# Performance work log

Measured on AMD Instinct MI355X. Metric: run time of the kernel, lower is better.

The kernel has to match this reference:

```python
import jax, jax.numpy as jnp
import numpy as np

BN_EPS = 1e-5


def segment_mean(data, ids, num_segments):
    s = jax.ops.segment_sum(data, ids, num_segments=num_segments)
    cnt = jax.ops.segment_sum(jnp.ones((data.shape[0], 1), data.dtype), ids,
                              num_segments=num_segments)
    return s / jnp.maximum(cnt, 1.0)


def sage_conv(x_src, x_dst, src, dst, Wl, Wr, b):
    # PyG SAGEConv (aggr='mean', root_weight=True):
    # out = lin_l(mean_j x_src[j]) + lin_r(x_dst)
    agg = segment_mean(x_src[src], dst, x_dst.shape[0])
    return agg @ Wl + b + x_dst @ Wr


def simple_conv(x, src, dst, W1, b1, W2, b2):
    # message = MLP(concat[x_j, x_i - x_j]); mean aggregation at target i
    x_j = x[src]
    x_i = x[dst]
    tmp = jnp.concatenate([x_j, x_i - x_j], axis=1)          # [E, 2d]
    msg = jax.nn.elu(tmp @ W1 + b1) @ W2 + b2                 # [E, d_out]
    return segment_mean(msg, dst, x.shape[0])


def batch_norm(x, gamma, beta):
    # training-mode BatchNorm1d: biased batch stats
    mu = jnp.mean(x, axis=0)
    var = jnp.mean(jnp.square(x - mu), axis=0)
    return gamma * (x - mu) * jax.lax.rsqrt(var + BN_EPS) + beta


def setup_inputs() -> dict:
    key = jax.random.key(0)
    ks = jax.random.split(key, 12)
    n_stu, n_item, d = 100000, 20000, 128
    e_r, e_p = 500000, 300000
    s = 1.0 / np.sqrt(d)
    s2 = 1.0 / np.sqrt(2 * d)
    return {
        "x_student": jax.random.normal(ks[0], (n_stu, d), jnp.float32),
        "x_item": jax.random.normal(ks[1], (n_item, d), jnp.float32),
        "responds_src": jax.random.randint(ks[2], (e_r,), 0, n_stu),
        "responds_dst": jax.random.randint(ks[3], (e_r,), 0, n_item),
        "preceeds_src": jax.random.randint(ks[4], (e_p,), 0, n_stu),
        "preceeds_dst": jax.random.randint(ks[5], (e_p,), 0, n_stu),
        "sage_it_Wl": jax.random.normal(ks[6], (d, d), jnp.float32) * s,
        "sage_it_Wr": jax.random.normal(ks[7], (d, d), jnp.float32) * s,
        "sage_it_b": jnp.zeros((d,), jnp.float32),
        "sage_st_Wl": jax.random.normal(ks[8], (d, d), jnp.float32) * s,
        "sage_st_Wr": jax.random.normal(ks[9], (d, d), jnp.float32) * s,
        "sage_st_b": jnp.zeros((d,), jnp.float32),
        "sc_W1": jax.random.normal(ks[10], (2 * d, d), jnp.float32) * s2,
        "sc_b1": jnp.zeros((d,), jnp.float32),
        "sc_W2": jax.random.normal(ks[11], (d, d), jnp.float32) * s,
        "sc_b2": jnp.zeros((d,), jnp.float32),
        "bn_item_g": jnp.ones((d,), jnp.float32),
        "bn_item_b": jnp.zeros((d,), jnp.float32),
        "bn_stu_g": jnp.ones((d,), jnp.float32),
        "bn_stu_b": jnp.zeros((d,), jnp.float32),
    }


def reference(x_student, x_item, responds_src, responds_dst, preceeds_src,
              preceeds_dst, sage_it_Wl, sage_it_Wr, sage_it_b, sage_st_Wl,
              sage_st_Wr, sage_st_b, sc_W1, sc_b1, sc_W2, sc_b2, bn_item_g,
              bn_item_b, bn_stu_g, bn_stu_b):
    # ('student','responds','item'): SAGEConv -> item
    item_out = sage_conv(x_student, x_item, responds_src, responds_dst,
                         sage_it_Wl, sage_it_Wr, sage_it_b)
    # ('item','rev_responds','student'): SAGEConv on reversed edges -> student
    stu_sage = sage_conv(x_item, x_student, responds_dst, responds_src,
                         sage_st_Wl, sage_st_Wr, sage_st_b)
    # ('student','preceeds','student'): SimpleConv -> student
    stu_simple = simple_conv(x_student, preceeds_src, preceeds_dst,
                             sc_W1, sc_b1, sc_W2, sc_b2)
    # HeteroConv aggr='mean' over the two student contributions
    stu_out = (stu_sage + stu_simple) * 0.5

    item_out = batch_norm(jax.nn.elu(item_out), bn_item_g, bn_item_b)
    stu_out = batch_norm(jax.nn.elu(stu_out), bn_stu_g, bn_stu_b)
    return item_out, stu_out
```

## Files before the change

### kernel.cpp

```cpp
#include <hip/hip_runtime.h>
#include <hip/hip_bf16.h>
#include <math.h>

#define D 128

typedef unsigned short ushort_t;
typedef __attribute__((ext_vector_type(8))) short bf16x8;
typedef __attribute__((ext_vector_type(4))) float f32x4;

__device__ __forceinline__ float bf2f(unsigned short u) {
    union { unsigned int i; float f; } c; c.i = ((unsigned int)u) << 16; return c.f;
}
__device__ __forceinline__ unsigned short f2bf(float f) {
    union { float f; unsigned int i; } c; c.f = f;
    unsigned int x = c.i + 0x7fffu + ((c.i >> 16) & 1u);
    return (unsigned short)(x >> 16);
}
__device__ __forceinline__ float eluf(float x) { return x > 0.f ? x : (expf(x) - 1.f); }

__device__ __forceinline__ void gload_lds16(const void* g, void* l) {
    __builtin_amdgcn_global_load_lds(
        (const __attribute__((address_space(1))) unsigned int*)g,
        (__attribute__((address_space(3))) unsigned int*)l, 16, 0, 0);
}

__global__ __launch_bounds__(256) void k_setup(
    const float* __restrict__ sc_W1, const float* __restrict__ it_Wl,
    const float* __restrict__ it_Wr, const float* __restrict__ st_Wl,
    const float* __restrict__ st_Wr, const float* __restrict__ sc_W2,
    ushort_t* __restrict__ Bpack,
    const float* __restrict__ x_item, ushort_t* __restrict__ xi16, int nxi,
    const int* __restrict__ rdst, const int* __restrict__ rsrc,
    const int* __restrict__ pdst, int* __restrict__ counts,
    int e_r, int e_p, int n_item, int n_stu, int PACKB, int CVTB) {
    int bx = blockIdx.x, tid = threadIdx.x;
    if (bx < PACKB) {
        int t = bx * 256 + tid;
        int s = t >> 14;
        int r = t & 16383;
        int j = r & 7;
        int lane = (r >> 3) & 63;
        int tile = r >> 9;
        int nt = tile & 7, kc = tile >> 3;
        int n = nt * 16 + (lane & 15);
        int k = kc * 32 + ((lane >> 4) << 3) + j;
        float v;
        switch (s) {
            case 0: v = sc_W1[k * 128 + n] - sc_W1[(128 + k) * 128 + n]; break;
            case 1: v = sc_W1[(128 + k) * 128 + n]; break;
            case 2: v = it_Wl[k * 128 + n]; break;
            case 3: v = it_Wr[k * 128 + n]; break;
            case 4: v = st_Wl[k * 128 + n]; break;
            case 5: v = st_Wr[k * 128 + n]; break;
            default: v = sc_W2[k * 128 + n]; break;
        }
        Bpack[t] = f2bf(v);
    } else if (bx < PACKB + CVTB) {
        int base = (bx - PACKB) * 2048 + tid * 8;
        if (base < nxi) {
            const float* g = x_item + base;
            float4 a0 = ((const float4*)g)[0];
            float4 a1 = ((const float4*)g)[1];
            ushort4 u0 = { f2bf(a0.x), f2bf(a0.y), f2bf(a0.z), f2bf(a0.w) };
            ushort4 u1 = { f2bf(a1.x), f2bf(a1.y), f2bf(a1.z), f2bf(a1.w) };
            *(ushort4*)(xi16 + base)     = u0;
            *(ushort4*)(xi16 + base + 4) = u1;
        }
    } else {
        int i = (bx - PACKB - CVTB) * 256 + tid;
        int total = 2 * e_r + e_p;
        if (i >= total) return;
        if (i < e_r)            atomicAdd(&counts[rdst[i]], 1);
        else if (i < 2 * e_r)   atomicAdd(&counts[n_item + rsrc[i - e_r]], 1);
        else                    atomicAdd(&counts[n_item + n_stu + pdst[i - 2 * e_r]], 1);
    }
}

__global__ __launch_bounds__(256) void k_scanA(const int* __restrict__ counts,
                                               int* __restrict__ bsums, int NN) {
    __shared__ int red[256];
    int tid = threadIdx.x;
    int base = blockIdx.x * 1024 + tid * 4;
    int s = 0;
    #pragma unroll
    for (int j = 0; j < 4; ++j) { int idx = base + j; if (idx < NN) s += counts[idx]; }
    red[tid] = s; __syncthreads();
    for (int off = 128; off; off >>= 1) {
        if (tid < off) red[tid] += red[tid + off];
        __syncthreads();
    }
    if (tid == 0) bsums[blockIdx.x] = red[0];
}

__global__ __launch_bounds__(256) void k_scanB(int* __restrict__ bsums, int nb) {
    __shared__ int wsum[4];
    int tid = threadIdx.x;
    int lane = tid & 63, w = tid >> 6;
    int v = (tid < nb) ? bsums[tid] : 0;
    int orig = v;
    #pragma unroll
    for (int off = 1; off < 64; off <<= 1) {
        int t = __shfl_up(v, off, 64);
        if (lane >= off) v += t;
    }
    if (lane == 63) wsum[w] = v;
    __syncthreads();
    int wo = 0;
    #pragma unroll
    for (int i = 0; i < 4; ++i) if (i < w) wo += wsum[i];
    if (tid < nb) bsums[tid] = wo + v - orig;
}

__global__ __launch_bounds__(256) void k_scanC(int* __restrict__ counts,
                                               const int* __restrict__ bsums,
                                               int* __restrict__ rowptr,
                                               int NN, int total) {
    __shared__ int wsum[4];
    int tid = threadIdx.x;
    int lane = tid & 63, w = tid >> 6;
    int base = blockIdx.x * 1024 + tid * 4;
    int c[4]; int ls = 0;
    #pragma unroll
    for (int j = 0; j < 4; ++j) { int idx = base + j; c[j] = (idx < NN) ? counts[idx] : 0; ls += c[j]; }
    int v = ls;
    #pragma unroll
    for (int off = 1; off < 64; off <<= 1) {
        int t = __shfl_up(v, off, 64);
        if (lane >= off) v += t;
    }
    if (lane == 63) wsum[w] = v;
    __syncthreads();
    int wo = 0;
    #pragma unroll
    for (int i = 0; i < 4; ++i) if (i < w) wo += wsum[i];
    int run = bsums[blockIdx.x] + wo + (v - ls);
    #pragma unroll
    for (int j = 0; j < 4; ++j) {
        int idx = base + j;
        if (idx < NN) {
            rowptr[idx] = run; counts[idx] = run;
            if (idx == NN - 1) rowptr[NN] = total;
        }
        run += c[j];
    }
}

__global__ __launch_bounds__(256) void k_scatter(const int* __restrict__ rdst,
                                                 const int* __restrict__ rsrc,
                                                 const int* __restrict__ pdst,
                                                 const int* __restrict__ psrc,
                                                 int* __restrict__ cursor,
                                                 int* __restrict__ payload,
                                                 int e_r, int e_p, int n_item, int n_stu) {
    int i = blockIdx.x * 256 + threadIdx.x;
    int total = 2 * e_r + e_p;
    if (i >= total) return;
    int g, src;
    if (i < e_r)          { g = rdst[i];                        src = rsrc[i]; }
    else if (i < 2 * e_r) { int j = i - e_r; g = n_item + rsrc[j]; src = rdst[j]; }
    else                  { int j = i - 2 * e_r; g = n_item + n_stu + pdst[j]; src = psrc[j]; }
    int slot = atomicAdd(&cursor[g], 1);
    payload[slot] = src;
}

__global__ __launch_bounds__(256) void k_agg(const ushort_t* __restrict__ xs16,
                                             const ushort_t* __restrict__ xi16,
                                             const ushort_t* __restrict__ U,
                                             const ushort_t* __restrict__ V,
                                             const int* __restrict__ rowptr,
                                             const int* __restrict__ payload,
                                             float* __restrict__ agg_item,
                                             float* __restrict__ agg_stu,
                                             ushort_t* __restrict__ hm16,
                                             int n_item, int n_stu) {
    int t = blockIdx.x * 256 + threadIdx.x;
    int node = t >> 5;
    int lane = t & 31;
    int NN = n_item + 2 * n_stu;
    if (node >= NN) return;
    int p0 = rowptr[node], p1 = rowptr[node + 1];
    float inv = 1.0f / (float)max(p1 - p0, 1);
    float ax = 0.f, ay = 0.f, az = 0.f, aw = 0.f;
    if (node < n_item + n_stu) {
        const ushort_t* src = (node < n_item) ? xs16 : xi16;
        int p = p0;
        for (; p + 4 <= p1; p += 4) {
            int e0 = payload[p], e1 = payload[p + 1], e2 = payload[p + 2], e3 = payload[p + 3];
            ushort4 r0 = *(const ushort4*)(src + (size_t)e0 * D + lane * 4);
            ushort4 r1 = *(const ushort4*)(src + (size_t)e1 * D + lane * 4);
            ushort4 r2 = *(const ushort4*)(src + (size_t)e2 * D + lane * 4);
            ushort4 r3 = *(const ushort4*)(src + (size_t)e3 * D + lane * 4);
            ax += (bf2f(r0.x) + bf2f(r1.x)) + (bf2f(r2.x) + bf2f(r3.x));
            ay += (bf2f(r0.y) + bf2f(r1.y)) + (bf2f(r2.y) + bf2f(r3.y));
            az += (bf2f(r0.z) + bf2f(r1.z)) + (bf2f(r2.z) + bf2f(r3.z));
            aw += (bf2f(r0.w) + bf2f(r1.w)) + (bf2f(r2.w) + bf2f(r3.w));
        }
        for (; p < p1; ++p) {
            int e = payload[p];
            ushort4 r = *(const ushort4*)(src + (size_t)e * D + lane * 4);
            ax += bf2f(r.x); ay += bf2f(r.y); az += bf2f(r.z); aw += bf2f(r.w);
        }
        float4 o = { ax * inv, ay * inv, az * inv, aw * inv };
        if (node < n_item) *(float4*)(agg_item + (size_t)node * D + lane * 4) = o;
        else               *(float4*)(agg_stu + (size_t)(node - n_item) * D + lane * 4) = o;
    } else {
        int n = node - n_item - n_stu;
        ushort4 vu = *(const ushort4*)(V + (size_t)n * D + lane * 4);
        float vx = bf2f(vu.x), vy = bf2f(vu.y), vz = bf2f(vu.z), vw = bf2f(vu.w);
        int p = p0;
        for (; p + 4 <= p1; p += 4) {
            int e0 = payload[p], e1 = payload[p + 1], e2 = payload[p + 2], e3 = payload[p + 3];
            ushort4 r0 = *(const ushort4*)(U + (size_t)e0 * D + lane * 4);
            ushort4 r1 = *(const ushort4*)(U + (size_t)e1 * D + lane * 4);
            ushort4 r2 = *(const ushort4*)(U + (size_t)e2 * D + lane * 4);
            ushort4 r3 = *(const ushort4*)(U + (size_t)e3 * D + lane * 4);
            ax += (eluf(bf2f(r0.x) + vx) + eluf(bf2f(r1.x) + vx)) + (eluf(bf2f(r2.x) + vx) + eluf(bf2f(r3.x) + vx));
            ay += (eluf(bf2f(r0.y) + vy) + eluf(bf2f(r1.y) + vy)) + (eluf(bf2f(r2.y) + vy) + eluf(bf2f(r3.y) + vy));
            az += (eluf(bf2f(r0.z) + vz) + eluf(bf2f(r1.z) + vz)) + (eluf(bf2f(r2.z) + vz) + eluf(bf2f(r3.z) + vz));
            aw += (eluf(bf2f(r0.w) + vw) + eluf(bf2f(r1.w) + vw)) + (eluf(bf2f(r2.w) + vw) + eluf(bf2f(r3.w) + vw));
        }
        for (; p < p1; ++p) {
            int e = payload[p];
            ushort4 r = *(const ushort4*)(U + (size_t)e * D + lane * 4);
            ax += eluf(bf2f(r.x) + vx); ay += eluf(bf2f(r.y) + vy);
            az += eluf(bf2f(r.z) + vz); aw += eluf(bf2f(r.w) + vw);
        }
        ushort4 o = { f2bf(ax * inv), f2bf(ay * inv), f2bf(az * inv), f2bf(aw * inv) };
        *(ushort4*)(hm16 + (size_t)n * D + lane * 4) = o;
    }
}

__device__ __forceinline__ void gemm_core(const void* A0, int t0,
                                          const void* A1, int t1,
                                          const void* A2, int t2,
                                          int nsrc, const ushort_t* Bp0,
                                          int M, int row0, ushort_t* xside,
                                          short* As, short* Bs, f32x4 (&acc)[4][4]) {
    const int tid = threadIdx.x;
    const int wave = tid >> 6, lane = tid & 63;
    const int mh = wave >> 1, nh = wave & 1;
    const int q = lane >> 4, l15 = lane & 15;
    #pragma unroll
    for (int i = 0; i < 4; ++i)
        #pragma unroll
        for (int j = 0; j < 4; ++j) acc[i][j] = (f32x4){0.f, 0.f, 0.f, 0.f};

    for (int s = 0; s < nsrc; ++s) {
        const void* Ap = (s == 0) ? A0 : ((s == 1) ? A1 : A2);
        const int at = (s == 0) ? t0 : ((s == 1) ? t1 : t2);
        const ushort_t* Bp = Bp0 + s * 16384;
        for (int h = 0; h < 2; ++h) {
            __syncthreads();
            #pragma unroll
            for (int it = 0; it < 4; ++it) {
                int tile = wave * 4 + it;
                int mt = tile & 7, kc = tile >> 3;
                int row = row0 + mt * 16 + l15;
                if (row >= M) row = M - 1;
                int k = h * 64 + kc * 32 + (q << 3);
                if (at == 0) {
                    const float* g = (const float*)Ap + (size_t)row * D + k;
                    float4 a0 = ((const float4*)g)[0];
                    float4 a1 = ((const float4*)g)[1];
                    ushort4 u0 = { f2bf(a0.x), f2bf(a0.y), f2bf(a0.z), f2bf(a0.w) };
                    ushort4 u1 = { f2bf(a1.x), f2bf(a1.y), f2bf(a1.z), f2bf(a1.w) };
                    short* dst = &As[tile * 512 + lane * 8];
                    *(ushort4*)dst       = u0;
                    *(ushort4*)(dst + 4) = u1;
                    if (xside) {
                        ushort_t* o = xside + (size_t)row * D + k;
                        *(ushort4*)o       = u0;
                        *(ushort4*)(o + 4) = u1;
                    }
                } else {
                    gload_lds16((const ushort_t*)Ap + (size_t)row * D + k, &As[tile * 512]);
                }
            }
            const ushort_t* bsrc = Bp + h * 8192;
            #pragma unroll
            for (int it = 0; it < 4; ++it) {
                int tile = wave * 4 + it;
                gload_lds16(bsrc + tile * 512 + lane * 8, &Bs[tile * 512]);
            }
            __syncthreads();
            #pragma unroll
            for (int kc = 0; kc < 2; ++kc) {
                bf16x8 a[4], b[4];
                #pragma unroll
                for (int i = 0; i < 4; ++i)
                    a[i] = *(bf16x8*)&As[(kc * 8 + mh * 4 + i) * 512 + lane * 8];
                #pragma unroll
                for (int j = 0; j < 4; ++j)
                    b[j] = *(bf16x8*)&Bs[(kc * 8 + nh * 4 + j) * 512 + lane * 8];
                #pragma unroll
                for (int i = 0; i < 4; ++i)
                    #pragma unroll
                    for (int j = 0; j < 4; ++j)
                        acc[i][j] = __builtin_amdgcn_mfma_f32_16x16x32_bf16(a[i], b[j], acc[i][j], 0, 0, 0);
            }
        }
    }
}

__global__ __launch_bounds__(256) void k_gemmUV(const float* __restrict__ xs,
                                                const ushort_t* __restrict__ Bpack,
                                                const float* __restrict__ b1,
                                                ushort_t* __restrict__ U,
                                                ushort_t* __restrict__ V,
                                                ushort_t* __restrict__ xs16, int M) {
    __shared__ short As[8192];
    __shared__ short Bs[8192];
    const int y = blockIdx.y;
    f32x4 acc[4][4];
    gemm_core(xs, 0, nullptr, 0, nullptr, 0, 1, Bpack + y * 16384, M,
              blockIdx.x * 128, y == 0 ? xs16 : nullptr, As, Bs, acc);
    const int tid = threadIdx.x;
    const int wave = tid >> 6, lane = tid & 63;
    const int mh = wave >> 1, nh = wave & 1;
    const int q = lane >> 4, l15 = lane & 15;
    ushort_t* C = (y == 0) ? U : V;
    float bv[4];
    #pragma unroll
    for (int j = 0; j < 4; ++j) {
        int col = (nh * 4 + j) * 16 + l15;
        bv[j] = (y == 0) ? b1[col] : 0.f;
    }
    const int row0 = blockIdx.x * 128;
    #pragma unroll
    for (int i = 0; i < 4; ++i) {
        int rowbase = row0 + (mh * 4 + i) * 16 + (q << 2);
        #pragma unroll
        for (int r = 0; r < 4; ++r) {
            int row = rowbase + r;
            if (row >= M) continue;
            #pragma unroll
            for (int j = 0; j < 4; ++j) {
                int col = (nh * 4 + j) * 16 + l15;
                C[(size_t)row * D + col] = f2bf(acc[i][j][r] + bv[j]);
            }
        }
    }
}

__global__ __launch_bounds__(256) void k_gemmF(const float* __restrict__ agg_item,
                                               const ushort_t* __restrict__ xi16,
                                               const float* __restrict__ agg_stu,
                                               const ushort_t* __restrict__ xs16,
                                               const ushort_t* __restrict__ hm16,
                                               const ushort_t* __restrict__ Bpack,
                                               const float* __restrict__ it_b,
                                               const float* __restrict__ st_b,
                                               const float* __restrict__ sc_b2,
                                               const int* __restrict__ rowptrS,
                                               float* __restrict__ out_item,
                                               float* __restrict__ out_stu,
                                               float* __restrict__ stats,
                                               int n_item, int n_stu, int gs_item) {
    __shared__ short As[8192];
    __shared__ short Bs[8192];
    const int bx = blockIdx.x;
    const bool is_item = bx < gs_item;
    f32x4 acc[4][4];
    int M, row0;
    const float* bias;
    float scale;
    float* C;
    float* st;
    if (is_item) {
        M = n_item; row0 = bx * 128;
        gemm_core(agg_item, 0, xi16, 1, nullptr, 1, 2, Bpack + 2 * 16384, M, row0,
                  nullptr, As, Bs, acc);
        bias = it_b; scale = 1.f; C = out_item; st = stats;
    } else {
        M = n_stu; row0 = (bx - gs_item) * 128;
        gemm_core(agg_stu, 0, xs16, 1, hm16, 1, 3, Bpack + 4 * 16384, M, row0,
                  nullptr, As, Bs, acc);
        bias = st_b; scale = 0.5f; C = out_stu; st = stats + 256;
    }
    const int tid = threadIdx.x;
    const int wave = tid >> 6, lane = tid & 63;
    const int mh = wave >> 1, nh = wave & 1;
    const int q = lane >> 4, l15 = lane & 15;
    float* sred = (float*)As;
    __syncthreads();
    sred[tid] = 0.f;
    __syncthreads();
    float bv[4], b2v[4];
    #pragma unroll
    for (int j = 0; j < 4; ++j) {
        int col = (nh * 4 + j) * 16 + l15;
        bv[j]  = bias[col];
        b2v[j] = is_item ? 0.f : sc_b2[col];
    }
    float ps[4] = {0.f, 0.f, 0.f, 0.f}, pq[4] = {0.f, 0.f, 0.f, 0.f};
    #pragma unroll
    for (int i = 0; i < 4; ++i) {
        int rowbase = row0 + (mh * 4 + i) * 16 + (q << 2);
        #pragma unroll
        for (int r = 0; r < 4; ++r) {
            int row = rowbase + r;
            if (row >= M) continue;
            float g = 0.f;
            if (!is_item) g = (rowptrS[row + 1] - rowptrS[row]) > 0 ? 1.f : 0.f;
            #pragma unroll
            for (int j = 0; j < 4; ++j) {
                int col = (nh * 4 + j) * 16 + l15;
                float v = acc[i][j][r] + bv[j];
                if (!is_item) v += g * b2v[j];
                v *= scale;
                v = eluf(v);
                C[(size_t)row * D + col] = v;
                ps[j] += v; pq[j] += v * v;
            }
        }
    }
    #pragma unroll
    for (int j = 0; j < 4; ++j) {
        int col = (nh * 4 + j) * 16 + l15;
        atomicAdd(&sred[col], ps[j]);
        atomicAdd(&sred[128 + col], pq[j]);
    }
    __syncthreads();
    atomicAdd(&st[tid], sred[tid]);
}

__global__ __launch_bounds__(256) void k_bnapply(float* __restrict__ out_item,
                                                 float* __restrict__ out_stu,
                                                 const float* __restrict__ stats,
                                                 const float* __restrict__ g_i,
                                                 const float* __restrict__ b_i,
                                                 const float* __restrict__ g_s,
                                                 const float* __restrict__ b_s,
                                                 int n_item, int n_stu, int blkItem) {
    int bx = blockIdx.x;
    float* X; const float* st; const float* gamma; const float* beta;
    float invM; int idx;
    if (bx < blkItem) {
        X = out_item; st = stats; gamma = g_i; beta = b_i;
        invM = 1.f / (float)n_item; idx = bx * 1024 + threadIdx.x * 4;
    } else {
        X = out_stu; st = stats + 256; gamma = g_s; beta = b_s;
        invM = 1.f / (float)n_stu; idx = (bx - blkItem) * 1024 + threadIdx.x * 4;
    }
    int c = idx & 127;
    float4 x = *(float4*)(X + idx);
    float o[4];
    #pragma unroll
    for (int j = 0; j < 4; ++j) {
        float mu = st[c + j] * invM;
        float var = st[128 + c + j] * invM - mu * mu;
        float v = (j == 0) ? x.x : (j == 1) ? x.y : (j == 2) ? x.z : x.w;
        o[j] = gamma[c + j] * (v - mu) * rsqrtf(var + 1e-5f) + beta[c + j];
    }
    float4 ov = { o[0], o[1], o[2], o[3] };
    *(float4*)(X + idx) = ov;
}

extern "C" void kernel_launch(void* const* d_in, const int* in_sizes, int n_in,
                              void* d_out, int out_size, void* d_ws, size_t ws_size,
                              hipStream_t stream) {
    const float* x_stu   = (const float*)d_in[0];
    const float* x_item  = (const float*)d_in[1];
    const int*   rsrc    = (const int*)d_in[2];
    const int*   rdst    = (const int*)d_in[3];
    const int*   psrc    = (const int*)d_in[4];
    const int*   pdst    = (const int*)d_in[5];
    const float* it_Wl   = (const float*)d_in[6];
    const float* it_Wr   = (const float*)d_in[7];
    const float* it_b    = (const float*)d_in[8];
    const float* st_Wl   = (const float*)d_in[9];
    const float* st_Wr   = (const float*)d_in[10];
    const float* st_b    = (const float*)d_in[11];
    const float* sc_W1   = (const float*)d_in[12];
    const float* sc_b1   = (const float*)d_in[13];
    const float* sc_W2   = (const float*)d_in[14];
    const float* sc_b2   = (const float*)d_in[15];
    const float* bn_it_g = (const float*)d_in[16];
    const float* bn_it_b = (const float*)d_in[17];
    const float* bn_st_g = (const float*)d_in[18];
    const float* bn_st_b = (const float*)d_in[19];

    const int n_stu  = in_sizes[0] / D;
    const int n_item = in_sizes[1] / D;
    const int e_r    = in_sizes[2];
    const int e_p    = in_sizes[4];
    const int NN     = n_item + 2 * n_stu;
    const int tot_e  = 2 * e_r + e_p;
    const int nb     = (NN + 1023) / 1024;

    char* w = (char*)d_ws;
    size_t off = 0;
    auto alloc = [&](size_t bytes) { char* p = w + off; off = (off + bytes + 255) & ~(size_t)255; return p; };
    int*      counts = (int*)alloc((size_t)NN * 4);
    float*    stats  = (float*)alloc(512 * 4);
    int*      rowptr = (int*)alloc((size_t)(NN + 1) * 4);
    int*      bsums  = (int*)alloc(256 * 4);
    int*      payload= (int*)alloc((size_t)tot_e * 4);
    ushort_t* U      = (ushort_t*)alloc((size_t)n_stu * D * 2);
    ushort_t* V      = (ushort_t*)alloc((size_t)n_stu * D * 2);
    ushort_t* xs16   = (ushort_t*)alloc((size_t)n_stu * D * 2);
    ushort_t* xi16   = (ushort_t*)alloc((size_t)n_item * D * 2);
    ushort_t* hm16   = (ushort_t*)alloc((size_t)n_stu * D * 2);
    ushort_t* Bpack  = (ushort_t*)alloc(7 * 16384 * 2);
    (void)ws_size; (void)n_in; (void)out_size;

    float* out_item = (float*)d_out;
    float* out_stu  = (float*)d_out + (size_t)n_item * D;

    size_t zspan = (char*)(stats + 512) - (char*)counts;
    hipMemsetAsync(counts, 0, zspan, stream);

    const int PACKB = (7 * 16384) / 256;
    const int nxi   = n_item * D;
    const int CVTB  = (nxi + 2047) / 2048;
    const int HISTB = (tot_e + 255) / 256;
    k_setup<<<PACKB + CVTB + HISTB, 256, 0, stream>>>(
        sc_W1, it_Wl, it_Wr, st_Wl, st_Wr, sc_W2, Bpack,
        x_item, xi16, nxi, rdst, rsrc, pdst, counts,
        e_r, e_p, n_item, n_stu, PACKB, CVTB);

    k_scanA<<<nb, 256, 0, stream>>>(counts, bsums, NN);
    k_scanB<<<1, 256, 0, stream>>>(bsums, nb);
    k_scanC<<<nb, 256, 0, stream>>>(counts, bsums, rowptr, NN, tot_e);
    k_scatter<<<HISTB, 256, 0, stream>>>(rdst, rsrc, pdst, psrc, counts, payload,
                                         e_r, e_p, n_item, n_stu);

    const int gs_stu  = (n_stu + 127) / 128;
    const int gs_item = (n_item + 127) / 128;

    k_gemmUV<<<dim3(gs_stu, 2), 256, 0, stream>>>(x_stu, Bpack, sc_b1, U, V, xs16, n_stu);

    k_agg<<<((size_t)NN * 32 + 255) / 256, 256, 0, stream>>>(
        xs16, xi16, U, V, rowptr, payload, out_item, out_stu, hm16, n_item, n_stu);

    k_gemmF<<<gs_item + gs_stu, 256, 0, stream>>>(
        out_item, xi16, out_stu, xs16, hm16, Bpack, it_b, st_b, sc_b2,
        rowptr + n_item + n_stu, out_item, out_stu, stats, n_item, n_stu, gs_item);

    const int blkItem = (n_item * D) / 1024;
    const int blkStu  = (n_stu * D) / 1024;
    k_bnapply<<<blkItem + blkStu, 256, 0, stream>>>(
        out_item, out_stu, stats, bn_it_g, bn_it_b, bn_st_g, bn_st_b,
        n_item, n_stu, blkItem);
}
```

Before: 483.8 us.

## Replace global atomic CSR build with two-level bucketed counting sort

Builds the CSR by first histogramming edges into 1024-node buckets using shared-memory atomics, scanning only the bucket counts, then depositing packed (local node, source) records into per-bucket FIFO segments and finishing each bucket's local sort in shared memory. This removes the per-node global atomic histogram, the three-kernel multi-block scan and the scattered global atomic cursor writes. In exchange it adds a FIFO buffer, an extra pass over edges, and packing that assumes source ids fit in 17 bits and NN fits in 256 buckets.

```diff
diff --git a/kernel.cpp b/kernel.cpp
--- a/kernel.cpp
+++ b/kernel.cpp
@@ -31,8 +31,9 @@
     ushort_t* __restrict__ Bpack,
     const float* __restrict__ x_item, ushort_t* __restrict__ xi16, int nxi,
     const int* __restrict__ rdst, const int* __restrict__ rsrc,
-    const int* __restrict__ pdst, int* __restrict__ counts,
+    const int* __restrict__ pdst, int* __restrict__ bucketCnt,
     int e_r, int e_p, int n_item, int n_stu, int PACKB, int CVTB) {
+    __shared__ int cnt[256];
     int bx = blockIdx.x, tid = threadIdx.x;
     if (bx < PACKB) {
         int t = bx * 256 + tid;
@@ -67,36 +68,34 @@
             *(ushort4*)(xi16 + base + 4) = u1;
         }
     } else {
-        int i = (bx - PACKB - CVTB) * 256 + tid;
+        int base = (bx - PACKB - CVTB) * 2048;
         int total = 2 * e_r + e_p;
-        if (i >= total) return;
-        if (i < e_r)            atomicAdd(&counts[rdst[i]], 1);
-        else if (i < 2 * e_r)   atomicAdd(&counts[n_item + rsrc[i - e_r]], 1);
-        else                    atomicAdd(&counts[n_item + n_stu + pdst[i - 2 * e_r]], 1);
-    }
-}
-
-__global__ __launch_bounds__(256) void k_scanA(const int* __restrict__ counts,
-                                               int* __restrict__ bsums, int NN) {
-    __shared__ int red[256];
-    int tid = threadIdx.x;
-    int base = blockIdx.x * 1024 + tid * 4;
-    int s = 0;
-    #pragma unroll
-    for (int j = 0; j < 4; ++j) { int idx = base + j; if (idx < NN) s += counts[idx]; }
-    red[tid] = s; __syncthreads();
-    for (int off = 128; off; off >>= 1) {
-        if (tid < off) red[tid] += red[tid + off];
+        cnt[tid] = 0;
         __syncthreads();
-    }
-    if (tid == 0) bsums[blockIdx.x] = red[0];
-}
-
-__global__ __launch_bounds__(256) void k_scanB(int* __restrict__ bsums, int nb) {
+        #pragma unroll
+        for (int j = 0; j < 8; ++j) {
+            int i = base + j * 256 + tid;
+            if (i < total) {
+                int g;
+                if (i < e_r)            g = rdst[i];
+                else if (i < 2 * e_r)   g = n_item + rsrc[i - e_r];
+                else                    g = n_item + n_stu + pdst[i - 2 * e_r];
+                atomicAdd(&cnt[g >> 10], 1);
+            }
+        }
+        __syncthreads();
+        if (cnt[tid] > 0) atomicAdd(&bucketCnt[tid], cnt[tid]);
+    }
+}
+
+__global__ __launch_bounds__(256) void k_bscan(const int* __restrict__ bucketCnt,
+                                               int* __restrict__ bucketOff,
+                                               int* __restrict__ bucketCursor,
+                                               int NB, int tot_e,
+                                               int* __restrict__ rowptr, int NN) {
     __shared__ int wsum[4];
-    int tid = threadIdx.x;
-    int lane = tid & 63, w = tid >> 6;
-    int v = (tid < nb) ? bsums[tid] : 0;
+    int tid = threadIdx.x, lane = tid & 63, w = tid >> 6;
+    int v = (tid < NB) ? bucketCnt[tid] : 0;
     int orig = v;
     #pragma unroll
     for (int off = 1; off < 64; off <<= 1) {
@@ -108,59 +107,119 @@
     int wo = 0;
     #pragma unroll
     for (int i = 0; i < 4; ++i) if (i < w) wo += wsum[i];
-    if (tid < nb) bsums[tid] = wo + v - orig;
-}
-
-__global__ __launch_bounds__(256) void k_scanC(int* __restrict__ counts,
-                                               const int* __restrict__ bsums,
-                                               int* __restrict__ rowptr,
-                                               int NN, int total) {
-    __shared__ int wsum[4];
-    int tid = threadIdx.x;
-    int lane = tid & 63, w = tid >> 6;
-    int base = blockIdx.x * 1024 + tid * 4;
-    int c[4]; int ls = 0;
-    #pragma unroll
-    for (int j = 0; j < 4; ++j) { int idx = base + j; c[j] = (idx < NN) ? counts[idx] : 0; ls += c[j]; }
-    int v = ls;
-    #pragma unroll
-    for (int off = 1; off < 64; off <<= 1) {
-        int t = __shfl_up(v, off, 64);
-        if (lane >= off) v += t;
-    }
-    if (lane == 63) wsum[w] = v;
-    __syncthreads();
-    int wo = 0;
-    #pragma unroll
-    for (int i = 0; i < 4; ++i) if (i < w) wo += wsum[i];
-    int run = bsums[blockIdx.x] + wo + (v - ls);
-    #pragma unroll
-    for (int j = 0; j < 4; ++j) {
-        int idx = base + j;
-        if (idx < NN) {
-            rowptr[idx] = run; counts[idx] = run;
-            if (idx == NN - 1) rowptr[NN] = total;
-        }
-        run += c[j];
-    }
-}
-
-__global__ __launch_bounds__(256) void k_scatter(const int* __restrict__ rdst,
+    int excl = wo + v - orig;
+    if (tid < NB) { bucketOff[tid] = excl; bucketCursor[tid] = excl; }
+    if (tid == 0) { bucketOff[NB] = tot_e; rowptr[NN] = tot_e; }
+}
+
+__global__ __launch_bounds__(256) void k_deposit(const int* __restrict__ rdst,
                                                  const int* __restrict__ rsrc,
                                                  const int* __restrict__ pdst,
                                                  const int* __restrict__ psrc,
-                                                 int* __restrict__ cursor,
-                                                 int* __restrict__ payload,
+                                                 unsigned int* __restrict__ fifo,
+                                                 int* __restrict__ bucketCursor,
                                                  int e_r, int e_p, int n_item, int n_stu) {
-    int i = blockIdx.x * 256 + threadIdx.x;
+    __shared__ unsigned int recs[2048];
+    __shared__ int cnt[256], excl[256], cur[256], scn[256];
+    int tid = threadIdx.x;
+    int base = blockIdx.x * 2048;
     int total = 2 * e_r + e_p;
-    if (i >= total) return;
-    int g, src;
-    if (i < e_r)          { g = rdst[i];                        src = rsrc[i]; }
-    else if (i < 2 * e_r) { int j = i - e_r; g = n_item + rsrc[j]; src = rdst[j]; }
-    else                  { int j = i - 2 * e_r; g = n_item + n_stu + pdst[j]; src = psrc[j]; }
-    int slot = atomicAdd(&cursor[g], 1);
-    payload[slot] = src;
+    unsigned int myrec[8]; int myb[8];
+    cnt[tid] = 0;
+    __syncthreads();
+    #pragma unroll
+    for (int j = 0; j < 8; ++j) {
+        int i = base + j * 256 + tid;
+        if (i < total) {
+            int g, s;
+            if (i < e_r)          { g = rdst[i];                          s = rsrc[i]; }
+            else if (i < 2 * e_r) { int q = i - e_r; g = n_item + rsrc[q]; s = rdst[q]; }
+            else                  { int q = i - 2 * e_r; g = n_item + n_stu + pdst[q]; s = psrc[q]; }
+            int b = g >> 10;
+            myrec[j] = ((unsigned int)(g & 1023) << 17) | (unsigned int)s;
+            myb[j] = b;
+            atomicAdd(&cnt[b], 1);
+        } else myb[j] = -1;
+    }
+    __syncthreads();
+    scn[tid] = cnt[tid];
+    __syncthreads();
+    for (int s1 = 1; s1 < 256; s1 <<= 1) {
+        int v = (tid >= s1) ? scn[tid - s1] : 0;
+        __syncthreads();
+        scn[tid] += v;
+        __syncthreads();
+    }
+    excl[tid] = scn[tid] - cnt[tid];
+    cur[tid] = excl[tid];
+    __syncthreads();
+    #pragma unroll
+    for (int j = 0; j < 8; ++j) {
+        if (myb[j] >= 0) {
+            int p = atomicAdd(&cur[myb[j]], 1);
+            recs[p] = myrec[j];
+        }
+    }
+    __syncthreads();
+    int wave = tid >> 6, lane = tid & 63;
+    for (int b = wave; b < 256; b += 4) {
+        int c = cnt[b];
+        if (c == 0) continue;
+        int gbase;
+        if (lane == 0) gbase = atomicAdd(&bucketCursor[b], c);
+        gbase = __shfl(gbase, 0);
+        int lb = excl[b];
+        for (int k = lane; k < c; k += 64) fifo[gbase + k] = recs[lb + k];
+    }
+}
+
+__global__ __launch_bounds__(256) void k_finalize(const unsigned int* __restrict__ fifo,
+                                                  const int* __restrict__ bucketOff,
+                                                  int* __restrict__ rowptr,
+                                                  int* __restrict__ payload,
+                                                  int NN) {
+    __shared__ int hist[1024];
+    __shared__ int scn[256];
+    __shared__ int cursor[1024];
+    int b = blockIdx.x, tid = threadIdx.x;
+    int nbase = b << 10;
+    int f0 = bucketOff[b], f1 = bucketOff[b + 1];
+    #pragma unroll
+    for (int j = 0; j < 4; ++j) hist[tid * 4 + j] = 0;
+    __syncthreads();
+    for (int p = f0 + tid; p < f1; p += 256)
+        atomicAdd(&hist[fifo[p] >> 17], 1);
+    __syncthreads();
+    int h0 = hist[tid * 4], h1 = hist[tid * 4 + 1], h2 = hist[tid * 4 + 2], h3 = hist[tid * 4 + 3];
+    int tsum = h0 + h1 + h2 + h3;
+    scn[tid] = tsum;
+    __syncthreads();
+    for (int s1 = 1; s1 < 256; s1 <<= 1) {
+        int v = (tid >= s1) ? scn[tid - s1] : 0;
+        __syncthreads();
+        scn[tid] += v;
+        __syncthreads();
+    }
+    int e0 = f0 + scn[tid] - tsum;
+    int e1 = e0 + h0, e2 = e1 + h1, e3 = e2 + h2;
+    cursor[tid * 4] = e0; cursor[tid * 4 + 1] = e1;
+    cursor[tid * 4 + 2] = e2; cursor[tid * 4 + 3] = e3;
+    int node = nbase + tid * 4;
+    if (node + 3 < NN) {
+        int4 rp = { e0, e1, e2, e3 };
+        *(int4*)(rowptr + node) = rp;
+    } else {
+        if (node < NN)     rowptr[node]     = e0;
+        if (node + 1 < NN) rowptr[node + 1] = e1;
+        if (node + 2 < NN) rowptr[node + 2] = e2;
+        if (node + 3 < NN) rowptr[node + 3] = e3;
+    }
+    __syncthreads();
+    for (int p = f0 + tid; p < f1; p += 256) {
+        unsigned int r = fifo[p];
+        int pos = atomicAdd(&cursor[r >> 17], 1);
+        payload[pos] = (int)(r & 0x1FFFFu);
+    }
 }
 
 __global__ __launch_bounds__(256) void k_agg(const ushort_t* __restrict__ xs16,
@@ -486,16 +545,19 @@
     const int e_p    = in_sizes[4];
     const int NN     = n_item + 2 * n_stu;
     const int tot_e  = 2 * e_r + e_p;
-    const int nb     = (NN + 1023) / 1024;
+    const int NB     = (NN + 1023) / 1024;
+    const int EB     = (tot_e + 2047) / 2048;
 
     char* w = (char*)d_ws;
     size_t off = 0;
     auto alloc = [&](size_t bytes) { char* p = w + off; off = (off + bytes + 255) & ~(size_t)255; return p; };
-    int*      counts = (int*)alloc((size_t)NN * 4);
-    float*    stats  = (float*)alloc(512 * 4);
-    int*      rowptr = (int*)alloc((size_t)(NN + 1) * 4);
-    int*      bsums  = (int*)alloc(256 * 4);
-    int*      payload= (int*)alloc((size_t)tot_e * 4);
+    int*      bucketCnt    = (int*)alloc(256 * 4);
+    float*    stats        = (float*)alloc(512 * 4);
+    int*      bucketOff    = (int*)alloc(260 * 4);
+    int*      bucketCursor = (int*)alloc(256 * 4);
+    int*      rowptr       = (int*)alloc((size_t)(NN + 1) * 4);
+    unsigned int* fifo     = (unsigned int*)alloc((size_t)tot_e * 4);
+    int*      payload      = (int*)alloc((size_t)tot_e * 4);
     ushort_t* U      = (ushort_t*)alloc((size_t)n_stu * D * 2);
     ushort_t* V      = (ushort_t*)alloc((size_t)n_stu * D * 2);
     ushort_t* xs16   = (ushort_t*)alloc((size_t)n_stu * D * 2);
@@ -507,23 +569,21 @@
     float* out_item = (float*)d_out;
     float* out_stu  = (float*)d_out + (size_t)n_item * D;
 
-    size_t zspan = (char*)(stats + 512) - (char*)counts;
-    hipMemsetAsync(counts, 0, zspan, stream);
+    size_t zspan = (char*)(stats + 512) - (char*)bucketCnt;
+    hipMemsetAsync(bucketCnt, 0, zspan, stream);
 
     const int PACKB = (7 * 16384) / 256;
     const int nxi   = n_item * D;
     const int CVTB  = (nxi + 2047) / 2048;
-    const int HISTB = (tot_e + 255) / 256;
-    k_setup<<<PACKB + CVTB + HISTB, 256, 0, stream>>>(
+    k_setup<<<PACKB + CVTB + EB, 256, 0, stream>>>(
         sc_W1, it_Wl, it_Wr, st_Wl, st_Wr, sc_W2, Bpack,
-        x_item, xi16, nxi, rdst, rsrc, pdst, counts,
+        x_item, xi16, nxi, rdst, rsrc, pdst, bucketCnt,
         e_r, e_p, n_item, n_stu, PACKB, CVTB);
 
-    k_scanA<<<nb, 256, 0, stream>>>(counts, bsums, NN);
-    k_scanB<<<1, 256, 0, stream>>>(bsums, nb);
-    k_scanC<<<nb, 256, 0, stream>>>(counts, bsums, rowptr, NN, tot_e);
-    k_scatter<<<HISTB, 256, 0, stream>>>(rdst, rsrc, pdst, psrc, counts, payload,
-                                         e_r, e_p, n_item, n_stu);
+    k_bscan<<<1, 256, 0, stream>>>(bucketCnt, bucketOff, bucketCursor, NB, tot_e, rowptr, NN);
+    k_deposit<<<EB, 256, 0, stream>>>(rdst, rsrc, pdst, psrc, fifo, bucketCursor,
+                                      e_r, e_p, n_item, n_stu);
+    k_finalize<<<NB, 256, 0, stream>>>(fifo, bucketOff, rowptr, payload, NN);
 
     const int gs_stu  = (n_stu + 127) / 128;
     const int gs_item = (n_item + 127) / 128;
```

New measurement: 583.6 us. 20.6% more time.
